# Optimization experiments

Hardware: AMD Instinct MI355X
Metric: run time of the kernel (lower is better)

## Reference

```python
import jax, jax.numpy as jnp
import numpy as np

NUM_HEADS = 8
RMS_EPS = 1e-8


def rmsnorm(x, g):
    return x * jax.lax.rsqrt(jnp.mean(x * x, axis=-1, keepdims=True) + RMS_EPS) * g


def activation_quant(x):
    # per-token int8 absmax quant
    scale = 127.0 / jnp.clip(jnp.max(jnp.abs(x), axis=-1, keepdims=True), 1e-5)
    return jnp.clip(jnp.round(x * scale), -128, 127) / scale


def weight_quant(w):
    # ternary (1.58-bit) mean-absmax quant
    scale = 1.0 / jnp.clip(jnp.mean(jnp.abs(w)), 1e-5)
    return jnp.clip(jnp.round(w * scale), -1, 1) / scale


def bitlinear(x, w, g):
    # BitLinear: RMSNorm -> STE-quantized activation @ STE-quantized ternary weight
    xn = rmsnorm(x, g)
    xq = xn + jax.lax.stop_gradient(activation_quant(xn) - xn)
    wq = w + jax.lax.stop_gradient(weight_quant(w) - w)
    return xq @ wq.T


def _attention_pass(q_in, ctx, Wq, gq, Wkv, gkv, A, Bm, mag, Wp, gp):
    B, Nq, C = q_in.shape
    H = NUM_HEADS
    hd = C // H
    scale = hd ** -0.5
    q_proj = bitlinear(q_in, Wq, gq)                       # [B,Nq,C]
    delta = (q_in @ A.T) @ Bm.T                            # DoRA low-rank delta [B,Nq,C]
    q = q_proj.reshape(B, Nq, H, hd).transpose(0, 2, 1, 3)  # [B,H,Nq,hd]
    d = delta.reshape(B, Nq, H, hd).transpose(0, 2, 1, 3)
    q_final = q + mag * d                                  # mag: [1,H,1,1]
    kv = bitlinear(ctx, Wkv, gkv)                          # [B,Nc,2C]
    k, v = jnp.split(kv, 2, axis=-1)
    Nc = ctx.shape[1]
    k = k.reshape(B, Nc, H, hd).transpose(0, 2, 1, 3)
    v = v.reshape(B, Nc, H, hd).transpose(0, 2, 1, 3)
    scores = jnp.einsum('bhqd,bhkd->bhqk', q_final, k) * scale
    out = jnp.einsum('bhqk,bhkd->bhqd', jax.nn.softmax(scores, axis=-1), v)
    out = out.transpose(0, 2, 1, 3).reshape(B, Nq, C)
    return bitlinear(out, Wp, gp)


def setup_inputs() -> dict:
    key = jax.random.key(0)
    ks = jax.random.split(key, 20)
    B, Nx, Nc, D, R = 4, 4096, 1024, 512, 16
    H = NUM_HEADS

    def rn(k, shape, s=0.02):
        return jax.random.normal(k, shape, dtype=jnp.float32) * s

    return {
        'x': jax.random.normal(ks[0], (B, Nx, D), dtype=jnp.float32),
        'c': jax.random.normal(ks[1], (B, Nc, D), dtype=jnp.float32),
        # x-queries-on-c pass
        'W_qx': rn(ks[2], (D, D)), 'g_qx': jnp.ones((D,), jnp.float32),
        'W_kvc': rn(ks[3], (2 * D, D)), 'g_kvc': jnp.ones((D,), jnp.float32),
        'A_x': rn(ks[4], (R, D)), 'B_x': rn(ks[5], (D, R)),
        'mag_x': jnp.ones((1, H, 1, 1), jnp.float32),
        'W_px': rn(ks[6], (D, D)), 'g_px': jnp.ones((D,), jnp.float32),
        # c-queries-on-x pass
        'W_qc': rn(ks[7], (D, D)), 'g_qc': jnp.ones((D,), jnp.float32),
        'W_kvx': rn(ks[8], (2 * D, D)), 'g_kvx': jnp.ones((D,), jnp.float32),
        'A_c': rn(ks[9], (R, D)), 'B_c': rn(ks[10], (D, R)),
        'mag_c': jnp.ones((1, H, 1, 1), jnp.float32),
        'W_pc': rn(ks[11], (D, D)), 'g_pc': jnp.ones((D,), jnp.float32),
    }


def reference(x, c, W_qx, g_qx, W_kvc, g_kvc, A_x, B_x, mag_x, W_px, g_px,
              W_qc, g_qc, W_kvx, g_kvx, A_c, B_c, mag_c, W_pc, g_pc):
    x_out = x + _attention_pass(x, c, W_qx, g_qx, W_kvc, g_kvc, A_x, B_x, mag_x, W_px, g_px)
    c_out = c + _attention_pass(c, x, W_qc, g_qc, W_kvx, g_kvx, A_c, B_c, mag_c, W_pc, g_pc)
    return (x_out, c_out)
```

## Files before the change

kernel.cpp:

```cpp
#include <hip/hip_runtime.h>
#include <math.h>

#define DD 512
#define NHEAD 8
#define HDIM 64

typedef __bf16 bf16x8 __attribute__((ext_vector_type(8)));
typedef unsigned short u16x8 __attribute__((ext_vector_type(8)));
typedef float f32x4 __attribute__((ext_vector_type(4)));
typedef int i32x4 __attribute__((ext_vector_type(4)));
typedef signed char i8x8 __attribute__((ext_vector_type(8)));

#if __has_builtin(__builtin_amdgcn_exp2f)
#define EXP2F(x) __builtin_amdgcn_exp2f(x)
#else
#define EXP2F(x) exp2f(x)
#endif

#define QSCALE 0.18033688f

static __device__ __forceinline__ unsigned short f2bf(float f) {
    unsigned u = __builtin_bit_cast(unsigned, f);
    u += 0x7fffu + ((u >> 16) & 1u);
    return (unsigned short)(u >> 16);
}
static __device__ __forceinline__ float bf2f(unsigned short u) {
    return __builtin_bit_cast(float, (unsigned)u << 16);
}

static __device__ __forceinline__ float wsum32(const float* __restrict__ part, int mid) {
    int l = threadIdx.x & 63;
    float v = (l < 32) ? part[mid * 32 + l] : 0.f;
#pragma unroll
    for (int o = 16; o > 0; o >>= 1) v += __shfl_xor(v, o);
    return __shfl(v, 0);
}

#define GLOAD16(g, l)                                                          \
    __builtin_amdgcn_global_load_lds(                                          \
        (__attribute__((address_space(1))) void*)(g),                          \
        (__attribute__((address_space(3))) void*)(l), 16, 0, 0)

#define BSTEP(s, hc)                                                           \
    {                                                                          \
        _Pragma("unroll")                                                      \
        for (int i = 0; i < (hc); ++i) {                                       \
            float send = (lane & (s)) ? p[i] : p[i + (hc)];                    \
            float recv = __shfl_xor(send, (s));                                \
            p[i] = ((lane & (s)) ? p[i + (hc)] : p[i]) + recv;                 \
        }                                                                      \
    }

#define GEMM_KLOOP_I8(Aq, Wq, m0, n0)                                          \
    {                                                                          \
        _Pragma("unroll")                                                      \
        for (int i = 0; i < 2; ++i)                                            \
            GLOAD16(Aq + (size_t)((m0) + i * 128 + row_st) * 512 + chunk * 16, \
                    sA[0] + ((size_t)i * 512 + t) * 16);                       \
        GLOAD16(Wq + (size_t)((n0) + row_st) * 512 + chunk * 16,               \
                sB[0] + (size_t)t * 16);                                       \
        asm volatile("s_waitcnt vmcnt(0)" ::: "memory");                       \
        __syncthreads();                                                       \
        int cur = 0;                                                           \
        for (int k0 = 0; k0 < 512; k0 += 64) {                                 \
            if (k0 + 64 < 512) {                                               \
                _Pragma("unroll")                                              \
                for (int i = 0; i < 2; ++i)                                    \
                    GLOAD16(Aq + (size_t)((m0) + i * 128 + row_st) * 512 + k0 + 64 + chunk * 16, \
                            sA[cur ^ 1] + ((size_t)i * 512 + t) * 16);         \
                GLOAD16(Wq + (size_t)((n0) + row_st) * 512 + k0 + 64 + chunk * 16, \
                        sB[cur ^ 1] + (size_t)t * 16);                         \
            }                                                                  \
            i32x4 af[4], bfr[4];                                               \
            _Pragma("unroll")                                                  \
            for (int mt = 0; mt < 4; ++mt)                                     \
                af[mt] = *reinterpret_cast<const i32x4*>(                      \
                    &sA[cur][(wm * 64 + mt * 16 + lr) * 64 + lg * 16]);        \
            _Pragma("unroll")                                                  \
            for (int nt = 0; nt < 4; ++nt)                                     \
                bfr[nt] = *reinterpret_cast<const i32x4*>(                     \
                    &sB[cur][(wn * 64 + nt * 16 + lr) * 64 + lg * 16]);        \
            __builtin_amdgcn_s_setprio(1);                                     \
            _Pragma("unroll")                                                  \
            for (int mt = 0; mt < 4; ++mt)                                     \
                _Pragma("unroll")                                              \
                for (int nt = 0; nt < 4; ++nt)                                 \
                    acc[mt][nt] = __builtin_amdgcn_mfma_i32_16x16x64_i8(       \
                        af[mt], bfr[nt], acc[mt][nt], 0, 0, 0);                \
            __builtin_amdgcn_s_setprio(0);                                     \
            asm volatile("s_waitcnt vmcnt(0)" ::: "memory");                   \
            __syncthreads();                                                   \
            cur ^= 1;                                                          \
        }                                                                      \
    }

__global__ __launch_bounds__(256) void k_prep1(
    const float* __restrict__ W0, const float* __restrict__ W1,
    const float* __restrict__ W2, const float* __restrict__ W3,
    const float* __restrict__ W4, const float* __restrict__ W5,
    float* __restrict__ part,
    const float* __restrict__ x, const float* __restrict__ c,
    const float* __restrict__ g_qx, const float* __restrict__ g_kvx,
    const float* __restrict__ g_qc, const float* __restrict__ g_kvc,
    signed char* __restrict__ a_xq, signed char* __restrict__ a_xkv,
    signed char* __restrict__ a_cq, signed char* __restrict__ a_ckv,
    float* __restrict__ s_xq, float* __restrict__ s_xkv,
    float* __restrict__ s_cq, float* __restrict__ s_ckv,
    const float* __restrict__ A_x, const float* __restrict__ A_c,
    float* __restrict__ tmp_x, float* __restrict__ tmp_c) {
    int t = threadIdx.x;
    if (blockIdx.x < 192) {
        const float* Ws[6] = {W0, W1, W2, W3, W4, W5};
        const int cnt[6] = {262144, 524288, 262144, 262144, 524288, 262144};
        int mid = blockIdx.x >> 5, lb = blockIdx.x & 31;
        const float* W = Ws[mid];
        int n = cnt[mid];
        float s = 0.f;
        for (int i = lb * 256 + t; i < n; i += 32 * 256) s += fabsf(W[i]);
        __shared__ float red[4];
#pragma unroll
        for (int o = 32; o > 0; o >>= 1) s += __shfl_down(s, o);
        if ((t & 63) == 0) red[t >> 6] = s;
        __syncthreads();
        if (t == 0) part[blockIdx.x] = red[0] + red[1] + red[2] + red[3];
        return;
    }
    int w = t >> 6, lane = t & 63;
    int row = (int)(blockIdx.x - 192) * 4 + w;
    bool pc = (row >= 16384);
    int r = pc ? row - 16384 : row;
    const float* xr = (pc ? c : x) + (size_t)r * DD;
    const float* G1 = pc ? g_qc : g_qx;
    const float* G2 = pc ? g_kvc : g_kvx;
    signed char* O1 = pc ? a_cq : a_xq;
    signed char* O2 = pc ? a_ckv : a_xkv;
    float* S1 = pc ? s_cq : s_xq;
    float* S2 = pc ? s_ckv : s_xkv;
    const float* AM = pc ? A_c : A_x;
    float* TMP = pc ? tmp_c : tmp_x;

    float4 a = *(const float4*)(xr + lane * 8);
    float4 b = *(const float4*)(xr + lane * 8 + 4);
    float p[16];
#pragma unroll
    for (int cc = 0; cc < 16; ++cc) {
        const float4* ar = (const float4*)(AM + (size_t)cc * DD + lane * 8);
        float4 aa = ar[0], ab = ar[1];
        p[cc] = a.x*aa.x + a.y*aa.y + a.z*aa.z + a.w*aa.w
              + b.x*ab.x + b.y*ab.y + b.z*ab.z + b.w*ab.w;
    }
    BSTEP(1, 8) BSTEP(2, 4) BSTEP(4, 2) BSTEP(8, 1)
    p[0] += __shfl_xor(p[0], 16);
    p[0] += __shfl_xor(p[0], 32);
    if (lane < 16) {
        int cidx = ((lane & 1) << 3) | ((lane & 2) << 1) | ((lane & 4) >> 1) | ((lane & 8) >> 3);
        TMP[(size_t)r * 16 + cidx] = p[0];
    }
    float ss = a.x*a.x + a.y*a.y + a.z*a.z + a.w*a.w
             + b.x*b.x + b.y*b.y + b.z*b.z + b.w*b.w;
#pragma unroll
    for (int o = 32; o > 0; o >>= 1) ss += __shfl_xor(ss, o);
    float rn = 1.f / sqrtf(ss * (1.f / 512.f) + 1e-8f);
    const float* gs[2] = {G1, G2};
    signed char* os[2] = {O1, O2};
    float* scs[2] = {S1, S2};
#pragma unroll
    for (int pass = 0; pass < 2; ++pass) {
        float4 ga = *(const float4*)(gs[pass] + lane * 8);
        float4 gb = *(const float4*)(gs[pass] + lane * 8 + 4);
        float v[8] = {a.x*rn*ga.x, a.y*rn*ga.y, a.z*rn*ga.z, a.w*rn*ga.w,
                      b.x*rn*gb.x, b.y*rn*gb.y, b.z*rn*gb.z, b.w*rn*gb.w};
        float amax = 0.f;
#pragma unroll
        for (int i = 0; i < 8; ++i) amax = fmaxf(amax, fabsf(v[i]));
#pragma unroll
        for (int o = 32; o > 0; o >>= 1) amax = fmaxf(amax, __shfl_xor(amax, o));
        float mx = fmaxf(amax, 1e-5f);
        float scale = 127.f / mx;
        i8x8 qv;
#pragma unroll
        for (int i = 0; i < 8; ++i) {
            float tq = rintf(v[i] * scale);
            tq = fminf(fmaxf(tq, -128.f), 127.f);
            qv[i] = (signed char)(int)tq;
        }
        *reinterpret_cast<i8x8*>(os[pass] + (size_t)r * DD + lane * 8) = qv;
        if (lane == 0) scs[pass][r] = mx / 127.f;
    }
}

__global__ __launch_bounds__(256) void k_prep2(
    const float* __restrict__ W0, const float* __restrict__ W1,
    const float* __restrict__ W2, const float* __restrict__ W3,
    const float* __restrict__ W4, const float* __restrict__ W5,
    const float* __restrict__ part, signed char* __restrict__ Wq,
    const float* __restrict__ tmp_x, const float* __restrict__ tmp_c,
    const float* __restrict__ B_x, const float* __restrict__ B_c,
    unsigned short* __restrict__ qf1, unsigned short* __restrict__ qf2) {
    if (blockIdx.x < 8192) {
        int e = blockIdx.x * 256 + threadIdx.x;
        const float* Ws[6] = {W0, W1, W2, W3, W4, W5};
        int mid, base;
        if (e < 262144)       { mid = 0; base = 0; }
        else if (e < 786432)  { mid = 1; base = 262144; }
        else if (e < 1048576) { mid = 2; base = 786432; }
        else if (e < 1310720) { mid = 3; base = 1048576; }
        else if (e < 1835008) { mid = 4; base = 1310720; }
        else                  { mid = 5; base = 1835008; }
        float cnt = (mid == 1 || mid == 4) ? 524288.f : 262144.f;
        float mean = fmaxf(wsum32(part, mid) / cnt, 1e-5f);
        float sc = 1.f / mean;
        float t = rintf(Ws[mid][e - base] * sc);
        t = fminf(fmaxf(t, -1.f), 1.f);
        Wq[e] = (signed char)(int)t;
        return;
    }
    int idx = (int)(blockIdx.x - 8192) * 256 + threadIdx.x;
    int m2 = idx >> 9, n2 = idx & 511;
    const float* tr;
    const float* br;
    unsigned short* out;
    if (m2 < 16384) {
        tr = tmp_x + (size_t)m2 * 16; br = B_x + (size_t)n2 * 16; out = qf1 + idx;
    } else {
        tr = tmp_c + (size_t)(m2 - 16384) * 16; br = B_c + (size_t)n2 * 16;
        out = qf2 + (idx - 8388608);
    }
    const float4* t4 = (const float4*)tr;
    const float4* b4 = (const float4*)br;
    float acc = 0.f;
#pragma unroll
    for (int rr = 0; rr < 4; ++rr) {
        float4 ta = t4[rr], ba = b4[rr];
        acc += ta.x*ba.x + ta.y*ba.y + ta.z*ba.z + ta.w*ba.w;
    }
    *out = f2bf(acc);
}

__global__ __launch_bounds__(256) void k_rmsq_combine(
    const unsigned short* __restrict__ Op_a, const float* __restrict__ Lp_a,
    const float* __restrict__ g_a, signed char* __restrict__ out_a,
    float* __restrict__ sc_a,
    const unsigned short* __restrict__ Op_b, const float* __restrict__ Lp_b,
    const float* __restrict__ g_b, signed char* __restrict__ out_b,
    float* __restrict__ sc_b) {
    int w = threadIdx.x >> 6, lane = threadIdx.x & 63;
    int row = (int)blockIdx.x * 4 + w;
    bool pb = (row >= 16384);
    int r = pb ? row - 16384 : row;
    int S = pb ? 4 : 1;
    int lognq = pb ? 10 : 12;
    const unsigned short* Op = pb ? Op_b : Op_a;
    const float* Lp = pb ? Lp_b : Lp_a;
    const float* g  = pb ? g_b : g_a;
    signed char* out = pb ? out_b : out_a;
    float* a_inv = pb ? sc_b : sc_a;

    int Nq = 1 << lognq;
    int b = r >> lognq, q = r & (Nq - 1);
    int h = lane >> 3;
    float l = 0.f;
    float u[8] = {};
    for (int s = 0; s < S; ++s) {
        l += Lp[((size_t)(s * 4 + b) * 8 + h) * Nq + q];
        u16x8 ov = *reinterpret_cast<const u16x8*>(
            Op + ((size_t)(s * 4 + b) * Nq + q) * 512 + lane * 8);
#pragma unroll
        for (int i = 0; i < 8; ++i) u[i] += bf2f(ov[i]);
    }
    float invl = 1.f / l;
#pragma unroll
    for (int i = 0; i < 8; ++i) u[i] *= invl;
    float ss = 0.f;
#pragma unroll
    for (int i = 0; i < 8; ++i) ss += u[i] * u[i];
#pragma unroll
    for (int o = 32; o > 0; o >>= 1) ss += __shfl_xor(ss, o);
    float rn = 1.f / sqrtf(ss * (1.f / 512.f) + 1e-8f);
    float4 ga = *(const float4*)(g + lane * 8);
    float4 gb = *(const float4*)(g + lane * 8 + 4);
    float v[8] = {u[0]*rn*ga.x, u[1]*rn*ga.y, u[2]*rn*ga.z, u[3]*rn*ga.w,
                  u[4]*rn*gb.x, u[5]*rn*gb.y, u[6]*rn*gb.z, u[7]*rn*gb.w};
    float amax = 0.f;
#pragma unroll
    for (int i = 0; i < 8; ++i) amax = fmaxf(amax, fabsf(v[i]));
#pragma unroll
    for (int o = 32; o > 0; o >>= 1) amax = fmaxf(amax, __shfl_xor(amax, o));
    float mx = fmaxf(amax, 1e-5f);
    float scale = 127.f / mx;
    i8x8 qv;
#pragma unroll
    for (int i = 0; i < 8; ++i) {
        float tq = rintf(v[i] * scale);
        tq = fminf(fmaxf(tq, -128.f), 127.f);
        qv[i] = (signed char)(int)tq;
    }
    *reinterpret_cast<i8x8*>(out + (size_t)r * DD + lane * 8) = qv;
    if (lane == 0) a_inv[r] = mx / 127.f;
}

__global__ __launch_bounds__(512) void k_gemm_qkv(
    const signed char* __restrict__ a3_a, const signed char* __restrict__ a3_b,
    const signed char* __restrict__ w3_a, const signed char* __restrict__ w3_b,
    const float* __restrict__ ai3_a, const float* __restrict__ ai3_b,
    const float* __restrict__ mag_a, const float* __restrict__ mag_b,
    const unsigned short* __restrict__ dl_a, const unsigned short* __restrict__ dl_b,
    unsigned short* __restrict__ Qb_a, unsigned short* __restrict__ Qb_b,
    const signed char* __restrict__ a4_a, const signed char* __restrict__ a4_b,
    const signed char* __restrict__ w4_a, const signed char* __restrict__ w4_b,
    const float* __restrict__ ai4_a, const float* __restrict__ ai4_b,
    unsigned short* __restrict__ Kb_a, unsigned short* __restrict__ Kb_b,
    unsigned short* __restrict__ Vt_a, unsigned short* __restrict__ Vt_b,
    const float* __restrict__ part) {
    __shared__ __align__(16) unsigned char sA[2][256 * 64];
    __shared__ __align__(16) unsigned char sB[2][128 * 64];
    int bid = blockIdx.x;
    bool isQ = (bid >= 640);
    const signed char *Aq, *Wq;
    const float* a_inv;
    int m0, n0, logn, mid;
    float cnt;
    bool pb;
    if (!isQ) {
        int g = bid & 7, k = bid >> 3;
        n0 = (k & 7) * 128;
        int my = (k >> 3) * 8 + g;
        pb = my >= 16;
        m0 = (pb ? my - 16 : my) * 256;
        Aq = pb ? a4_b : a4_a;  Wq = pb ? w4_b : w4_a;
        a_inv = pb ? ai4_b : ai4_a;
        logn = pb ? 12 : 10;
        mid = pb ? 4 : 1; cnt = 524288.f;
    } else {
        int b2 = bid - 640;
        int g = b2 & 7, k = b2 >> 3;
        n0 = (k & 3) * 128;
        int my = (k >> 2) * 8 + g;
        pb = my >= 64;
        m0 = (pb ? my - 64 : my) * 256;
        Aq = pb ? a3_b : a3_a;  Wq = pb ? w3_b : w3_a;
        a_inv = pb ? ai3_b : ai3_a;
        logn = pb ? 10 : 12;
        mid = pb ? 3 : 0; cnt = 262144.f;
    }
    float wv = fmaxf(wsum32(part, mid) / cnt, 1e-5f);

    int t = threadIdx.x;
    int w = t >> 6, lane = t & 63;
    int wm = w >> 1, wn = w & 1;
    int lr = lane & 15, lg = lane >> 4;
    int row_st = t >> 2, chunk = t & 3;
    i32x4 acc[4][4] = {};

    GEMM_KLOOP_I8(Aq, Wq, m0, n0)

    if (!isQ) {
        unsigned short* OutB = pb ? Kb_b : Kb_a;
        unsigned short* OutB2 = pb ? Vt_b : Vt_a;
        const bool isV = (n0 >= 512);
        const int Nc = 1 << logn;
#pragma unroll
        for (int mt = 0; mt < 4; ++mt) {
            int mb = m0 + wm * 64 + mt * 16 + lg * 4;
            int b = mb >> logn, key = mb & (Nc - 1);
            float as_[4];
#pragma unroll
            for (int r = 0; r < 4; ++r) as_[r] = a_inv[mb + r] * wv;
#pragma unroll
            for (int nt = 0; nt < 4; ++nt) {
                int n = n0 + wn * 64 + nt * 16 + lr;
                int n2 = isV ? (n - 512) : n;
                int h = n2 >> 6, dd = n2 & 63;
                if (isV) {
                    int i0 = key & 31;
                    int keyp = (key & ~31) | (((i0 >> 2) & 3) * 8 + ((i0 >> 4) & 1) * 4);
                    ushort4 v;
                    v.x = f2bf((float)acc[mt][nt][0] * as_[0]);
                    v.y = f2bf((float)acc[mt][nt][1] * as_[1]);
                    v.z = f2bf((float)acc[mt][nt][2] * as_[2]);
                    v.w = f2bf((float)acc[mt][nt][3] * as_[3]);
                    *reinterpret_cast<ushort4*>(
                        OutB2 + ((size_t)(b * NHEAD + h) * 64 + dd) * Nc + keyp) = v;
                } else {
#pragma unroll
                    for (int r = 0; r < 4; ++r)
                        OutB[((size_t)(b * NHEAD + h) * Nc + key + r) * 64 + dd] =
                            f2bf((float)acc[mt][nt][r] * as_[r]);
                }
            }
        }
    } else {
        const float* Extra = pb ? mag_b : mag_a;
        const unsigned short* Dlt = pb ? dl_b : dl_a;
        unsigned short* OutB = pb ? Qb_b : Qb_a;
#pragma unroll
        for (int mt = 0; mt < 4; ++mt) {
#pragma unroll
            for (int r = 0; r < 4; ++r) {
                int m = m0 + wm * 64 + mt * 16 + lg * 4 + r;
                float as = a_inv[m] * wv;
                int b = m >> logn, q = m & ((1 << logn) - 1);
#pragma unroll
                for (int nt = 0; nt < 4; ++nt) {
                    int n = n0 + wn * 64 + nt * 16 + lr;
                    float dl = bf2f(Dlt[(size_t)m * 512 + n]);
                    float val = (float)acc[mt][nt][r] * as + Extra[n >> 6] * dl;
                    int h = n >> 6, d = n & 63;
                    OutB[((((size_t)(b * NHEAD + h)) << logn) + q) * 64 + d] =
                        f2bf(val * QSCALE);
                }
            }
        }
    }
}

__global__ __launch_bounds__(512) void k_gemm_out(
    const signed char* __restrict__ a_a, const signed char* __restrict__ a_b,
    const signed char* __restrict__ w_a, const signed char* __restrict__ w_b,
    const float* __restrict__ ai_a, const float* __restrict__ ai_b,
    const float* __restrict__ part,
    const float* __restrict__ Ex_a, const float* __restrict__ Ex_b,
    float* __restrict__ OF_a, float* __restrict__ OF_b) {
    __shared__ __align__(16) unsigned char sA[2][256 * 64];
    __shared__ __align__(16) unsigned char sB[2][128 * 64];
    int bid = blockIdx.x;
    int g = bid & 7, k = bid >> 3;
    int n0 = (k & 3) * 128;
    int my = (k >> 2) * 8 + g;
    bool pb = (my >= 64);
    int m0 = (pb ? my - 64 : my) * 256;
    const signed char* Aq = pb ? a_b : a_a;
    const signed char* Wq = pb ? w_b : w_a;
    const float* a_inv = pb ? ai_b : ai_a;
    const float* Extra = pb ? Ex_b : Ex_a;
    float* OutF = pb ? OF_b : OF_a;
    float wv = fmaxf(wsum32(part, pb ? 5 : 2) / 262144.f, 1e-5f);

    int t = threadIdx.x;
    int w = t >> 6, lane = t & 63;
    int wm = w >> 1, wn = w & 1;
    int lr = lane & 15, lg = lane >> 4;
    int row_st = t >> 2, chunk = t & 3;
    i32x4 acc[4][4] = {};

    GEMM_KLOOP_I8(Aq, Wq, m0, n0)

#pragma unroll
    for (int mt = 0; mt < 4; ++mt) {
#pragma unroll
        for (int r = 0; r < 4; ++r) {
            int m = m0 + wm * 64 + mt * 16 + lg * 4 + r;
            float as = a_inv[m] * wv;
#pragma unroll
            for (int nt = 0; nt < 4; ++nt) {
                int n = n0 + wn * 64 + nt * 16 + lr;
                size_t idx = (size_t)m * 512 + n;
                OutF[idx] = (float)acc[mt][nt][r] * as + Extra[idx];
            }
        }
    }
}

__global__ __launch_bounds__(512) void k_attn_mfma(
    const unsigned short* __restrict__ Qb_a, const unsigned short* __restrict__ Kb_a,
    const unsigned short* __restrict__ Vt_a, unsigned short* __restrict__ Op_a,
    float* __restrict__ Lp_a,
    const unsigned short* __restrict__ Qb_b, const unsigned short* __restrict__ Kb_b,
    const unsigned short* __restrict__ Vt_b, unsigned short* __restrict__ Op_b,
    float* __restrict__ Lp_b) {
    __shared__ unsigned short sK[2][64][72];
    __shared__ unsigned short sVt[2][64][72];
    int t = threadIdx.x;
    int w = t >> 6, lane = t & 63;
    int lr = lane & 15, lg = lane >> 4;

    int bid = blockIdx.x;
    bool pb = (bid < 512);
    int lb = pb ? bid : bid - 512;
    const unsigned short* Qb = pb ? Qb_b : Qb_a;
    const unsigned short* Kb = pb ? Kb_b : Kb_a;
    const unsigned short* Vt = pb ? Vt_b : Vt_a;
    unsigned short* Opart = pb ? Op_b : Op_a;
    float* Lpart = pb ? Lp_b : Lp_a;
    int Nq = pb ? 1024 : 4096;
    int Nc = pb ? 4096 : 1024;
    int S = pb ? 4 : 1;
    int LOGS = pb ? 2 : 0;
    int nqs = pb ? 2 : 4;

    int j = lb >> 3;
    int s = j & (S - 1);
    int j2 = j >> LOGS;
    int qblk = j2 & ((1 << nqs) - 1);
    int bh = ((lb & 7) << 2) | (j2 >> nqs);
    int b = bh >> 3, h = bh & 7;
    int q0 = qblk * 256 + w * 32;

    bf16x8 aq[2][2];
#pragma unroll
    for (int qt = 0; qt < 2; ++qt) {
        const unsigned short* qbase = Qb + ((size_t)bh * Nq + q0 + qt * 16 + lr) * 64 + lg * 8;
        aq[qt][0] = *reinterpret_cast<const bf16x8*>(qbase);
        aq[qt][1] = *reinterpret_cast<const bf16x8*>(qbase + 32);
    }

    u16x8 ou;
#pragma unroll
    for (int jj = 0; jj < 8; ++jj) ou[jj] = (lr == 0) ? 0x3F80 : 0;
    bf16x8 onesf = __builtin_bit_cast(bf16x8, ou);

    f32x4 o[2][4] = {};
    f32x4 osum[2] = {};

    const unsigned short* kglob = Kb + (size_t)bh * Nc * 64;
    const unsigned short* vglob = Vt + (size_t)bh * 64 * (size_t)Nc;

    int srow = t >> 3, sseg = t & 7;
    const unsigned short* kptr = kglob + (size_t)srow * 64 + sseg * 8;
    const unsigned short* vptr = vglob + (size_t)srow * Nc + sseg * 8;

    int kts = s * (Nc >> LOGS);
    int nt = (Nc >> LOGS) >> 6;

    bf16x8 rK = *reinterpret_cast<const bf16x8*>(kptr + (size_t)kts * 64);
    bf16x8 rV = *reinterpret_cast<const bf16x8*>(vptr + kts);
    *reinterpret_cast<bf16x8*>(&sK[0][srow][sseg * 8]) = rK;
    *reinterpret_cast<bf16x8*>(&sVt[0][srow][sseg * 8]) = rV;
    rK = *reinterpret_cast<const bf16x8*>(kptr + (size_t)(kts + 64) * 64);
    rV = *reinterpret_cast<const bf16x8*>(vptr + kts + 64);
    __syncthreads();

    int cur = 0;
    for (int ti = 0; ti < nt; ++ti) {
        if (ti + 1 < nt) {
            *reinterpret_cast<bf16x8*>(&sK[cur ^ 1][srow][sseg * 8]) = rK;
            *reinterpret_cast<bf16x8*>(&sVt[cur ^ 1][srow][sseg * 8]) = rV;
            if (ti + 2 < nt) {
                int knext = kts + (ti + 2) * 64;
                rK = *reinterpret_cast<const bf16x8*>(kptr + (size_t)knext * 64);
                rV = *reinterpret_cast<const bf16x8*>(vptr + knext);
            }
        }
#pragma unroll
        for (int half = 0; half < 2; ++half) {
            bf16x8 pa0, pa1;
#pragma unroll
            for (int ki = 0; ki < 2; ++ki) {
                int kt = half * 2 + ki;
                bf16x8 bk0 = *reinterpret_cast<const bf16x8*>(&sK[cur][kt * 16 + lr][lg * 8]);
                bf16x8 bk1 = *reinterpret_cast<const bf16x8*>(&sK[cur][kt * 16 + lr][32 + lg * 8]);
                f32x4 a0 = {}, a1 = {};
                __builtin_amdgcn_s_setprio(1);
                a0 = __builtin_amdgcn_mfma_f32_16x16x32_bf16(bk0, aq[0][0], a0, 0, 0, 0);
                a1 = __builtin_amdgcn_mfma_f32_16x16x32_bf16(bk0, aq[1][0], a1, 0, 0, 0);
                a0 = __builtin_amdgcn_mfma_f32_16x16x32_bf16(bk1, aq[0][1], a0, 0, 0, 0);
                a1 = __builtin_amdgcn_mfma_f32_16x16x32_bf16(bk1, aq[1][1], a1, 0, 0, 0);
                __builtin_amdgcn_s_setprio(0);
                const int hb = ki * 4;
#pragma unroll
                for (int r = 0; r < 4; ++r) {
                    pa0[hb + r] = (__bf16)EXP2F(a0[r]);
                    pa1[hb + r] = (__bf16)EXP2F(a1[r]);
                }
            }
            __builtin_amdgcn_s_setprio(1);
#pragma unroll
            for (int dt = 0; dt < 4; ++dt) {
                bf16x8 vb = *reinterpret_cast<const bf16x8*>(&sVt[cur][dt * 16 + lr][half * 32 + lg * 8]);
                o[0][dt] = __builtin_amdgcn_mfma_f32_16x16x32_bf16(pa0, vb, o[0][dt], 0, 0, 0);
                o[1][dt] = __builtin_amdgcn_mfma_f32_16x16x32_bf16(pa1, vb, o[1][dt], 0, 0, 0);
            }
            osum[0] = __builtin_amdgcn_mfma_f32_16x16x32_bf16(pa0, onesf, osum[0], 0, 0, 0);
            osum[1] = __builtin_amdgcn_mfma_f32_16x16x32_bf16(pa1, onesf, osum[1], 0, 0, 0);
            __builtin_amdgcn_s_setprio(0);
        }
        __syncthreads();
        cur ^= 1;
    }
    unsigned short* obase = Opart + ((size_t)(s * 4 + b) * Nq + q0) * 512 + h * 64;
#pragma unroll
    for (int qt = 0; qt < 2; ++qt)
#pragma unroll
        for (int dt = 0; dt < 4; ++dt)
#pragma unroll
            for (int r = 0; r < 4; ++r)
                obase[(size_t)(qt * 16 + lg * 4 + r) * 512 + dt * 16 + lr] = f2bf(o[qt][dt][r]);
    if (lr == 0) {
        float* lbase = Lpart + ((size_t)(s * 4 + b) * 8 + h) * Nq + q0;
#pragma unroll
        for (int qt = 0; qt < 2; ++qt)
#pragma unroll
            for (int r = 0; r < 4; ++r)
                lbase[qt * 16 + lg * 4 + r] = osum[qt][r];
    }
}

extern "C" void kernel_launch(void* const* d_in, const int* in_sizes, int n_in,
                              void* d_out, int out_size, void* d_ws, size_t ws_size,
                              hipStream_t stream) {
    const float* x     = (const float*)d_in[0];
    const float* c     = (const float*)d_in[1];
    const float* Wq_x  = (const float*)d_in[2];
    const float* g_qx  = (const float*)d_in[3];
    const float* Wkv_c = (const float*)d_in[4];
    const float* g_kvc = (const float*)d_in[5];
    const float* A_x   = (const float*)d_in[6];
    const float* B_x   = (const float*)d_in[7];
    const float* mag_x = (const float*)d_in[8];
    const float* Wp_x  = (const float*)d_in[9];
    const float* g_px  = (const float*)d_in[10];
    const float* Wq_c  = (const float*)d_in[11];
    const float* g_qc  = (const float*)d_in[12];
    const float* Wkv_x = (const float*)d_in[13];
    const float* g_kvx = (const float*)d_in[14];
    const float* A_c   = (const float*)d_in[15];
    const float* B_c   = (const float*)d_in[16];
    const float* mag_c = (const float*)d_in[17];
    const float* Wp_c  = (const float*)d_in[18];
    const float* g_pc  = (const float*)d_in[19];

    float* ws = (float*)d_ws;
    signed char* Wb = (signed char*)ws;
    const size_t Woff[6] = {0, 262144, 786432, 1048576, 1310720, 1835008};
    float* part  = ws + 1048576;
    float* sc_xq  = ws + 1049600;
    float* sc_xkv = sc_xq + 16384;
    float* sc_cq  = sc_xkv + 16384;
    float* sc_ckv = sc_cq + 4096;
    float* sc_o1  = sc_ckv + 4096;
    float* sc_o2  = sc_o1 + 16384;
    float* tmp_x  = ws + 1111040;
    float* tmp_c  = tmp_x + 262144;
    float* actblk = ws + 1438720;
    signed char* act_xq  = (signed char*)actblk;
    signed char* act_xkv = (signed char*)(actblk + 4194304);
    signed char* act_cq  = (signed char*)(actblk + 8388608);
    signed char* act_ckv = (signed char*)(actblk + 9437184);
    unsigned short* Opart1 = (unsigned short*)actblk;
    float* qf1_f  = ws + 11924480;
    unsigned short* Opart2 = (unsigned short*)qf1_f;
    float* qf2_f  = ws + 16118784;
    float* Qb1_f  = ws + 17167360;
    float* Qb2_f  = ws + 21361664;
    float* Kb1_f  = ws + 22410240;
    float* Vt1_f  = ws + 23458816;
    float* Kb2_f  = ws + 24507392;
    float* Vt2_f  = ws + 28701696;
    float* Lpart1 = ws + 32896000;
    float* Lpart2 = ws + 33027072;

    unsigned short* qf1 = (unsigned short*)qf1_f;
    unsigned short* qf2 = (unsigned short*)qf2_f;
    unsigned short* Qb1 = (unsigned short*)Qb1_f;
    unsigned short* Qb2 = (unsigned short*)Qb2_f;
    unsigned short* Kb1 = (unsigned short*)Kb1_f;
    unsigned short* Vt1 = (unsigned short*)Vt1_f;
    unsigned short* Kb2 = (unsigned short*)Kb2_f;
    unsigned short* Vt2 = (unsigned short*)Vt2_f;
    signed char* act_o1 = (signed char*)Qb1;
    signed char* act_o2 = (signed char*)Qb2;

    size_t need = (size_t)33158144 * sizeof(float);
    if (ws_size < need) return;

    float* outx = (float*)d_out;
    float* outc = outx + (size_t)4 * 4096 * 512;

    k_prep1<<<5312, 256, 0, stream>>>(Wq_x, Wkv_c, Wp_x, Wq_c, Wkv_x, Wp_c, part,
                                      x, c, g_qx, g_kvx, g_qc, g_kvc,
                                      act_xq, act_xkv, act_cq, act_ckv,
                                      sc_xq, sc_xkv, sc_cq, sc_ckv,
                                      A_x, A_c, tmp_x, tmp_c);
    k_prep2<<<49152, 256, 0, stream>>>(Wq_x, Wkv_c, Wp_x, Wq_c, Wkv_x, Wp_c, part, Wb,
                                       tmp_x, tmp_c, B_x, B_c, qf1, qf2);
    k_gemm_qkv<<<960, 512, 0, stream>>>(
        act_xq, act_cq, Wb + Woff[0], Wb + Woff[3], sc_xq, sc_cq,
        mag_x, mag_c, qf1, qf2, Qb1, Qb2,
        act_ckv, act_xkv, Wb + Woff[1], Wb + Woff[4], sc_ckv, sc_xkv,
        Kb1, Kb2, Vt1, Vt2, part);
    k_attn_mfma<<<1024, 512, 0, stream>>>(Qb1, Kb1, Vt1, Opart1, Lpart1,
                                          Qb2, Kb2, Vt2, Opart2, Lpart2);
    k_rmsq_combine<<<5120, 256, 0, stream>>>(Opart1, Lpart1, g_px, act_o1, sc_o1,
                                             Opart2, Lpart2, g_pc, act_o2, sc_o2);
    k_gemm_out<<<320, 512, 0, stream>>>(
        act_o1, act_o2, Wb + Woff[2], Wb + Woff[5], sc_o1, sc_o2, part,
        x, c, outx, outc);
}
```

Measured before the change: 235.9 us.

## Triple-buffer int8 GEMM k-loop with prefetch distance two and partial vmcnt waits

Changes the int8 MFMA GEMM k-loop from a double-buffered, full-drain pipeline to a three-slot LDS ring. Tiles are prefetched two steps ahead, and each step waits only for the oldest outstanding loads (vmcnt(3)) before a raw s_barrier. The goal is to keep global-to-LDS loads in flight across MFMA work instead of draining memory every iteration. LDS use per block grows by half, to 72KB, which may lower occupancy. A slot that was read in the previous step is overwritten by this step's prefetch, so correctness depends on the barrier ordering.

New measurement: 234.8 us (median of 2 runs). No clear change (-0.4%).

```diff
diff --git a/kernel.cpp b/kernel.cpp
--- a/kernel.cpp
+++ b/kernel.cpp
@@ -51,35 +51,36 @@
         }                                                                      \
     }
 
-#define GEMM_KLOOP_I8(Aq, Wq, m0, n0)                                          \
+#define ISSUE_TILE(Aq, Wq, m0, n0, k0, slot)                                   \
     {                                                                          \
         _Pragma("unroll")                                                      \
         for (int i = 0; i < 2; ++i)                                            \
-            GLOAD16(Aq + (size_t)((m0) + i * 128 + row_st) * 512 + chunk * 16, \
-                    sA[0] + ((size_t)i * 512 + t) * 16);                       \
-        GLOAD16(Wq + (size_t)((n0) + row_st) * 512 + chunk * 16,               \
-                sB[0] + (size_t)t * 16);                                       \
-        asm volatile("s_waitcnt vmcnt(0)" ::: "memory");                       \
-        __syncthreads();                                                       \
-        int cur = 0;                                                           \
-        for (int k0 = 0; k0 < 512; k0 += 64) {                                 \
-            if (k0 + 64 < 512) {                                               \
-                _Pragma("unroll")                                              \
-                for (int i = 0; i < 2; ++i)                                    \
-                    GLOAD16(Aq + (size_t)((m0) + i * 128 + row_st) * 512 + k0 + 64 + chunk * 16, \
-                            sA[cur ^ 1] + ((size_t)i * 512 + t) * 16);         \
-                GLOAD16(Wq + (size_t)((n0) + row_st) * 512 + k0 + 64 + chunk * 16, \
-                        sB[cur ^ 1] + (size_t)t * 16);                         \
-            }                                                                  \
+            GLOAD16(Aq + (size_t)((m0) + i * 128 + row_st) * 512 + (k0) + chunk * 16, \
+                    sA[slot] + ((size_t)i * 512 + t) * 16);                    \
+        GLOAD16(Wq + (size_t)((n0) + row_st) * 512 + (k0) + chunk * 16,        \
+                sB[slot] + (size_t)t * 16);                                    \
+    }
+
+#define GEMM_KLOOP_I8(Aq, Wq, m0, n0)                                          \
+    {                                                                          \
+        ISSUE_TILE(Aq, Wq, m0, n0, 0, 0)                                       \
+        ISSUE_TILE(Aq, Wq, m0, n0, 64, 1)                                      \
+        asm volatile("s_waitcnt vmcnt(3)" ::: "memory");                       \
+        __builtin_amdgcn_s_barrier();                                          \
+        _Pragma("unroll")                                                      \
+        for (int step = 0; step < 8; ++step) {                                 \
+            if (step + 2 < 8)                                                  \
+                ISSUE_TILE(Aq, Wq, m0, n0, (step + 2) * 64, (step + 2) % 3)    \
+            const int cs = step % 3;                                           \
             i32x4 af[4], bfr[4];                                               \
             _Pragma("unroll")                                                  \
             for (int mt = 0; mt < 4; ++mt)                                     \
                 af[mt] = *reinterpret_cast<const i32x4*>(                      \
-                    &sA[cur][(wm * 64 + mt * 16 + lr) * 64 + lg * 16]);        \
+                    &sA[cs][(wm * 64 + mt * 16 + lr) * 64 + lg * 16]);         \
             _Pragma("unroll")                                                  \
             for (int nt = 0; nt < 4; ++nt)                                     \
                 bfr[nt] = *reinterpret_cast<const i32x4*>(                     \
-                    &sB[cur][(wn * 64 + nt * 16 + lr) * 64 + lg * 16]);        \
+                    &sB[cs][(wn * 64 + nt * 16 + lr) * 64 + lg * 16]);         \
             __builtin_amdgcn_s_setprio(1);                                     \
             _Pragma("unroll")                                                  \
             for (int mt = 0; mt < 4; ++mt)                                     \
@@ -88,9 +89,13 @@
                     acc[mt][nt] = __builtin_amdgcn_mfma_i32_16x16x64_i8(       \
                         af[mt], bfr[nt], acc[mt][nt], 0, 0, 0);                \
             __builtin_amdgcn_s_setprio(0);                                     \
-            asm volatile("s_waitcnt vmcnt(0)" ::: "memory");                   \
-            __syncthreads();                                                   \
-            cur ^= 1;                                                          \
+            if (step < 7) {                                                    \
+                if (step < 6)                                                  \
+                    asm volatile("s_waitcnt vmcnt(3)" ::: "memory");           \
+                else                                                           \
+                    asm volatile("s_waitcnt vmcnt(0)" ::: "memory");           \
+                __builtin_amdgcn_s_barrier();                                  \
+            }                                                                  \
         }                                                                      \
     }
 
@@ -312,8 +317,8 @@
     unsigned short* __restrict__ Kb_a, unsigned short* __restrict__ Kb_b,
     unsigned short* __restrict__ Vt_a, unsigned short* __restrict__ Vt_b,
     const float* __restrict__ part) {
-    __shared__ __align__(16) unsigned char sA[2][256 * 64];
-    __shared__ __align__(16) unsigned char sB[2][128 * 64];
+    __shared__ __align__(16) unsigned char sA[3][256 * 64];
+    __shared__ __align__(16) unsigned char sB[3][128 * 64];
     int bid = blockIdx.x;
     bool isQ = (bid >= 640);
     const signed char *Aq, *Wq;
@@ -421,8 +426,8 @@
     const float* __restrict__ part,
     const float* __restrict__ Ex_a, const float* __restrict__ Ex_b,
     float* __restrict__ OF_a, float* __restrict__ OF_b) {
-    __shared__ __align__(16) unsigned char sA[2][256 * 64];
-    __shared__ __align__(16) unsigned char sB[2][128 * 64];
+    __shared__ __align__(16) unsigned char sA[3][256 * 64];
+    __shared__ __align__(16) unsigned char sB[3][128 * 64];
     int bid = blockIdx.x;
     int g = bid & 7, k = bid >> 3;
     int n0 = (k & 3) * 128;
```
